# Kernel optimization log

Hardware: AMD Instinct MI355X
Metric: run time of the kernel (lower is better)

Reference implementation:

```python
import jax, jax.numpy as jnp
import numpy as np

NUM_GROUPS = 32
EPS = 1e-6


def group_norm(x, gamma, beta):
    # x: [b, c, h, w]
    b, c, h, w = x.shape
    g = NUM_GROUPS
    xg = x.reshape(b, g, c // g, h, w)
    mean = xg.mean(axis=(2, 3, 4), keepdims=True)
    var = xg.var(axis=(2, 3, 4), keepdims=True)
    xn = ((xg - mean) * jax.lax.rsqrt(var + EPS)).reshape(b, c, h, w)
    return xn * gamma[None, :, None, None] + beta[None, :, None, None]


def conv1x1(x, w, b):
    # x: [b, c, h, w], w: [out_c, in_c], b: [out_c]
    return jnp.einsum('bchw,oc->bohw', x, w) + b[None, :, None, None]


def setup_inputs() -> dict:
    key = jax.random.key(0)
    ks = jax.random.split(key, 11)
    B, C, H, W = 4, 512, 64, 64
    s = 1.0 / np.sqrt(C)
    inp = {
        'x': jax.random.normal(ks[0], (B, C, H, W), dtype=jnp.float32),
        'gn_gamma': jnp.ones((C,), dtype=jnp.float32),
        'gn_beta': jnp.zeros((C,), dtype=jnp.float32),
        'wq': jax.random.normal(ks[1], (C, C), dtype=jnp.float32) * s,
        'bq': jax.random.normal(ks[2], (C,), dtype=jnp.float32) * 0.01,
        'wk': jax.random.normal(ks[3], (C, C), dtype=jnp.float32) * s,
        'bk': jax.random.normal(ks[4], (C,), dtype=jnp.float32) * 0.01,
        'wv': jax.random.normal(ks[5], (C, C), dtype=jnp.float32) * s,
        'bv': jax.random.normal(ks[6], (C,), dtype=jnp.float32) * 0.01,
        'wo': jax.random.normal(ks[7], (C, C), dtype=jnp.float32) * s,
        'bo': jax.random.normal(ks[8], (C,), dtype=jnp.float32) * 0.01,
    }
    return inp


def reference(x, gn_gamma, gn_beta, wq, bq, wk, bk, wv, bv, wo, bo):
    b, c, h, w = x.shape
    h_ = group_norm(x, gn_gamma, gn_beta)
    q = conv1x1(h_, wq, bq).reshape(b, c, h * w)  # [b, c, n]
    k = conv1x1(h_, wk, bk).reshape(b, c, h * w)
    v = conv1x1(h_, wv, bv).reshape(b, c, h * w)
    scale = jnp.asarray(c, x.dtype) ** -0.5
    # attn[b, i, j] = softmax_j(q_i . k_j * scale)
    attn = jax.nn.softmax(jnp.einsum('bci,bcj->bij', q, k) * scale, axis=-1)
    # A[b, c, i] = sum_j attn[b, i, j] * v[b, c, j]
    A = jnp.einsum('bij,bcj->bci', attn, v).reshape(b, c, h, w)
    A = conv1x1(A, wo, bo)
    # NOTE: the original module multiplies (not adds) the input by the attention output
    return x * A
```

## Files before the change

### kernel.cpp

```cpp
#include <hip/hip_runtime.h>
#include <hip/hip_bf16.h>
#include <stdint.h>

typedef __bf16 bf16x8 __attribute__((ext_vector_type(8)));
typedef __bf16 bf16x4 __attribute__((ext_vector_type(4)));
typedef float f32x4 __attribute__((ext_vector_type(4)));

__device__ __forceinline__ void gload_lds16(const __bf16* g, __bf16* l) {
  __builtin_amdgcn_global_load_lds(
      (const __attribute__((address_space(1))) void*)g,
      (__attribute__((address_space(3))) void*)l, 16, 0, 0);
}

__global__ __launch_bounds__(256) void cvt4_kernel(const float* __restrict__ s0,
                                                   const float* __restrict__ s1,
                                                   const float* __restrict__ s2,
                                                   const float* __restrict__ s3,
                                                   __bf16* __restrict__ dst) {
  int i = blockIdx.x * 256 + threadIdx.x;
  const float* srcs[4] = {s0, s1, s2, s3};
  int m = i >> 18;
  dst[i] = (__bf16)srcs[m][i & 262143];
}

__global__ __launch_bounds__(256) void biascat_kernel(const float* __restrict__ bq,
                                                      const float* __restrict__ bk,
                                                      float* __restrict__ bqk) {
  int i = blockIdx.x * 256 + threadIdx.x;
  bqk[i] = (i < 512) ? bq[i] : bk[i - 512];
}

__global__ __launch_bounds__(256) void gn1a_kernel(const float* __restrict__ x,
                                                   __bf16* __restrict__ xbf,
                                                   float2* __restrict__ part) {
  const int tid = threadIdx.x;
  const size_t base4 = ((size_t)blockIdx.x * 8192) >> 2;
  const float4* x4 = (const float4*)x;
  bf16x4* o4 = (bf16x4*)xbf;

  float s1 = 0.f, s2 = 0.f;
#pragma unroll
  for (int j = 0; j < 8; ++j) {
    float4 t = x4[base4 + tid + j * 256];
    s1 += t.x + t.y + t.z + t.w;
    s2 += t.x * t.x + t.y * t.y + t.z * t.z + t.w * t.w;
    bf16x4 o;
    o[0] = (__bf16)t.x; o[1] = (__bf16)t.y; o[2] = (__bf16)t.z; o[3] = (__bf16)t.w;
    o4[base4 + tid + j * 256] = o;
  }
#pragma unroll
  for (int off = 32; off; off >>= 1) {
    s1 += __shfl_xor(s1, off);
    s2 += __shfl_xor(s2, off);
  }
  __shared__ float r1[4], r2[4];
  if ((tid & 63) == 0) { r1[tid >> 6] = s1; r2[tid >> 6] = s2; }
  __syncthreads();
  if (tid == 0)
    part[blockIdx.x] = float2{r1[0] + r1[1] + r1[2] + r1[3],
                              r2[0] + r2[1] + r2[2] + r2[3]};
}

__global__ __launch_bounds__(512) void gn1b_kernel(const float2* __restrict__ part,
                                                   const float* __restrict__ gamma,
                                                   const float* __restrict__ beta,
                                                   float2* __restrict__ gmbt) {
  const int b = blockIdx.x;
  const int t = threadIdx.x;
  __shared__ float sm[32], si[32];
  if (t < 32) {
    float s1 = 0.f, s2 = 0.f;
#pragma unroll
    for (int j = 0; j < 8; ++j) {
      float2 p = part[(b * 32 + t) * 8 + j];
      s1 += p.x; s2 += p.y;
    }
    const float mean = s1 * (1.f / 65536.f);
    const float var = s2 * (1.f / 65536.f) - mean * mean;
    sm[t] = mean;
    si[t] = rsqrtf(var + 1e-6f);
  }
  __syncthreads();
  const int g = t >> 4;
  const float gm = gamma[t] * si[g];
  gmbt[b * 512 + t] = float2{gm, beta[t] - sm[g] * gm};
}

__global__ __launch_bounds__(256) void gn2_kernel(const __bf16* __restrict__ xbf,
                                                  const float2* __restrict__ gmbt,
                                                  __bf16* __restrict__ hnT) {
  const int b = blockIdx.z;
  const int c0 = blockIdx.y * 64;
  const int n0 = blockIdx.x * 64;
  const int t = threadIdx.x;
  __shared__ __bf16 tile[64][72];

  {
    const int row = t >> 2;
    const int col = (t & 3) * 16;
    const __bf16* src = xbf + ((size_t)(b * 512 + c0 + row)) * 4096 + n0 + col;
    bf16x8 u0 = *(const bf16x8*)src;
    bf16x8 u1 = *(const bf16x8*)(src + 8);
    *(bf16x8*)&tile[row][col] = u0;
    *(bf16x8*)&tile[row][col + 8] = u1;
  }
  __syncthreads();
  {
    const int nrow = t >> 2;
    const int cc = (t & 3) * 16;
    bf16x8 o0, o1;
#pragma unroll
    for (int j = 0; j < 16; ++j) {
      const int c = c0 + cc + j;
      float2 s = gmbt[b * 512 + c];
      float val = (float)tile[cc + j][nrow] * s.x + s.y;
      if (j < 8) o0[j] = (__bf16)val; else o1[j - 8] = (__bf16)val;
    }
    __bf16* dst = hnT + ((size_t)b * 4096 + n0 + nrow) * 512 + c0 + cc;
    *(bf16x8*)dst = o0;
    *(bf16x8*)(dst + 8) = o1;
  }
}

__global__ __launch_bounds__(256) void softmax_bf16_kernel(__bf16* __restrict__ S) {
  const int N = 4096;
  __bf16* rp = S + (size_t)blockIdx.x * N;
  const int tid = threadIdx.x;
  bf16x8 v0 = ((const bf16x8*)rp)[tid * 2];
  bf16x8 v1 = ((const bf16x8*)rp)[tid * 2 + 1];
  float f[16];
#pragma unroll
  for (int i = 0; i < 8; ++i) { f[i] = (float)v0[i]; f[8 + i] = (float)v1[i]; }

  float mx = -1e30f;
#pragma unroll
  for (int i = 0; i < 16; ++i) mx = fmaxf(mx, f[i]);
#pragma unroll
  for (int off = 32; off; off >>= 1) mx = fmaxf(mx, __shfl_xor(mx, off));
  __shared__ float redm[4];
  if ((tid & 63) == 0) redm[tid >> 6] = mx;
  __syncthreads();
  mx = fmaxf(fmaxf(redm[0], redm[1]), fmaxf(redm[2], redm[3]));

  float sum = 0.f;
#pragma unroll
  for (int i = 0; i < 16; ++i) {
    f[i] = __expf(f[i] - mx);
    sum += f[i];
  }
#pragma unroll
  for (int off = 32; off; off >>= 1) sum += __shfl_xor(sum, off);
  __shared__ float reds[4];
  if ((tid & 63) == 0) reds[tid >> 6] = sum;
  __syncthreads();
  sum = reds[0] + reds[1] + reds[2] + reds[3];
  const float invs = 1.0f / sum;

  bf16x8 o0, o1;
#pragma unroll
  for (int i = 0; i < 8; ++i) {
    o0[i] = (__bf16)(f[i] * invs);
    o1[i] = (__bf16)(f[8 + i] * invs);
  }
  ((bf16x8*)rp)[tid * 2] = o0;
  ((bf16x8*)rp)[tid * 2 + 1] = o1;
}

template <int BN, int BIAS>
__global__ __launch_bounds__(512) void gemm8p_kernel(
    const __bf16* __restrict__ A, int lda, long long sA,
    const __bf16* __restrict__ Bm, int ldb, long long sB,
    __bf16* __restrict__ Out, int ldo, long long sO,
    const float* __restrict__ bias, float scale, int K) {
  constexpr int NF = BN / 64;
  constexpr int NH = NF / 2;
  constexpr int BSLOT = BN * 32;
  __shared__ __bf16 sm[4 * 8192 + 4 * BSLOT];
  __bf16* smB = sm + 4 * 8192;

  const int gx = gridDim.x, gxy = gx * gridDim.y;
  const int nwg = gxy * gridDim.z;
  int bid = blockIdx.x + gx * blockIdx.y + gxy * blockIdx.z;
  bid = (bid & 7) * (nwg >> 3) + (bid >> 3);
  const int bz = bid / gxy;
  const int rem = bid - bz * gxy;
  const int by = rem / gx, bx = rem - by * gx;
  const int tm0 = by * 256, tn0 = bx * BN;

  const int t = threadIdx.x;
  const int lane = t & 63, wid = t >> 6;
  const int wr = wid >> 2, wc = wid & 3;

  const __bf16* Az = A + (size_t)bz * sA;
  const __bf16* Bz = Bm + (size_t)bz * sB;

  const int scol = ((t & 3) * 8) ^ (((t >> 3) & 3) * 8);
  const __bf16* gA0 = Az + (size_t)(tm0 + (t >> 2)) * lda + scol;
  const __bf16* gA1 = gA0 + (size_t)128 * lda;
  const __bf16* gB0 = Bz + (size_t)(tn0 + (t >> 2)) * ldb + scol;
  const __bf16* gB1 = gB0 + (size_t)128 * ldb;
  __bf16* dA = sm + t * 8;
  __bf16* dB = smB + t * 8;

  auto stageA = [&](int ko, int sl) {
    gload_lds16(gA0 + ko, dA + sl * 8192);
    gload_lds16(gA1 + ko, dA + sl * 8192 + 4096);
  };
  auto stageB = [&](int ko, int sl) {
    gload_lds16(gB0 + ko, dB + sl * BSLOT);
    if constexpr (BN == 256) gload_lds16(gB1 + ko, dB + sl * BSLOT + 4096);
  };
  auto vmw = [&] {
    if constexpr (BN == 256) asm volatile("s_waitcnt vmcnt(8)" ::: "memory");
    else                     asm volatile("s_waitcnt vmcnt(6)" ::: "memory");
  };

  const int lr = lane & 15;
  const int kb = ((lane >> 4) * 16) ^ ((lr & 6) << 3);
  const __bf16* rdA = sm + (((wr * 128 + lr) * 64 + kb) >> 1);
  const __bf16* rdB = smB + (((wc * (BN / 4) + lr) * 64 + kb) >> 1);

  f32x4 acc[8][NF];
#pragma unroll
  for (int m = 0; m < 8; ++m)
#pragma unroll
    for (int n = 0; n < NF; ++n) acc[m][n] = f32x4{0.f, 0.f, 0.f, 0.f};
  bf16x8 av[8];

  auto rdAfr = [&](int sl) {
#pragma unroll
    for (int m = 0; m < 8; ++m)
      av[m] = *(const bf16x8*)(rdA + sl * 8192 + m * 512);
  };
  auto mmaPh = [&](int sl, int nh) {
    bf16x8 bv[NH];
#pragma unroll
    for (int j = 0; j < NH; ++j)
      bv[j] = *(const bf16x8*)(rdB + sl * BSLOT + (nh * NH + j) * 512);
    __builtin_amdgcn_s_barrier();
    __builtin_amdgcn_s_setprio(1);
#pragma unroll
    for (int m = 0; m < 8; ++m)
#pragma unroll
      for (int j = 0; j < NH; ++j)
        acc[m][nh * NH + j] = __builtin_amdgcn_mfma_f32_16x16x32_bf16(
            av[m], bv[j], acc[m][nh * NH + j], 0, 0, 0);
    __builtin_amdgcn_s_setprio(0);
    __builtin_amdgcn_s_barrier();
  };

  const int NT = K >> 6;
  const int NIT = NT >> 1;

  stageA(0, 0); stageB(0, 0); stageA(32, 1); stageB(32, 1);
  stageA(64, 2); stageB(64, 2);
  vmw();
  __builtin_amdgcn_s_barrier();

  for (int it = 0; it < NIT - 1; ++it) {
    const int kt = it * 2;
    const int k0 = kt * 64;
    rdAfr(0); stageA(k0 + 96, 3);          mmaPh(0, 0);
    stageB(k0 + 96, 3); vmw();             mmaPh(0, 1);
    rdAfr(1); stageA(k0 + 128, 0);         mmaPh(1, 0);
    stageB(k0 + 128, 0); vmw();            mmaPh(1, 1);
    rdAfr(2); stageA(k0 + 160, 1);         mmaPh(2, 0);
    stageB(k0 + 160, 1); vmw();            mmaPh(2, 1);
    rdAfr(3); stageA(k0 + 192, 2);         mmaPh(3, 0);
    stageB(k0 + 192, 2); vmw();            mmaPh(3, 1);
  }
  {
    const int k0 = (NT - 2) * 64;
    rdAfr(0); stageA(k0 + 96, 3);          mmaPh(0, 0);
    stageB(k0 + 96, 3); vmw();             mmaPh(0, 1);
    rdAfr(1);                              mmaPh(1, 0);
    if constexpr (BN == 256) asm volatile("s_waitcnt vmcnt(4)" ::: "memory");
    else                     asm volatile("s_waitcnt vmcnt(3)" ::: "memory");
    mmaPh(1, 1);
    rdAfr(2);                              mmaPh(2, 0);
    if constexpr (BN == 256) asm volatile("s_waitcnt vmcnt(2)" ::: "memory");
    else                     asm volatile("s_waitcnt vmcnt(1)" ::: "memory");
    mmaPh(2, 1);
    rdAfr(3);                              mmaPh(3, 0);
    mmaPh(3, 1);
  }

  const int q4 = (lane >> 4) * 4;
  const int wnb = tn0 + wc * (BN / 4);
  float bcol[NF];
#pragma unroll
  for (int n = 0; n < NF; ++n) bcol[n] = BIAS ? bias[wnb + n * 16 + lr] : 0.f;
#pragma unroll
  for (int m = 0; m < 8; ++m) {
#pragma unroll
    for (int r = 0; r < 4; ++r) {
      const int row = tm0 + wr * 128 + m * 16 + q4 + r;
      __bf16* orow = Out + (size_t)bz * sO + (size_t)row * ldo + wnb + lr;
#pragma unroll
      for (int n = 0; n < NF; ++n)
        orow[n * 16] = (__bf16)(acc[m][n][r] * scale + bcol[n]);
    }
  }
}

template <int EPI, int BIAS>
__global__ __launch_bounds__(256) void gemm_lds_kernel(
    const __bf16* __restrict__ A, int lda, long long sA,
    const __bf16* __restrict__ Bm, int ldb, long long sB,
    void* __restrict__ Out, int ldo, long long sO,
    const float* __restrict__ bias, const __bf16* __restrict__ xmul,
    long long sX, float scale, int K) {
  __shared__ __bf16 sTa[2][128 * 32];
  __shared__ __bf16 sTb[2][128 * 32];

  const int gx = gridDim.x, gxy = gx * gridDim.y;
  const int nwg = gxy * gridDim.z;
  int bid = blockIdx.x + gx * blockIdx.y + gxy * blockIdx.z;
  if ((nwg & 7) == 0) bid = (bid & 7) * (nwg >> 3) + (bid >> 3);
  const int bz = bid / gxy;
  const int rem = bid - bz * gxy;
  const int by = rem / gx;
  const int bx = rem - by * gx;

  const int tid = threadIdx.x;
  const int lane = tid & 63;
  const int wid = tid >> 6;
  const int wr = wid >> 1, wc = wid & 1;
  const int tm0 = by * 128, tn0 = bx * 128;
  const int lr = lane & 15, lk = (lane >> 4) * 8;

  const int ch0 = wid * 2;
  const int srow = lane >> 2;
  const int scol = (lane & 3) * 8;
  const __bf16* gA0 = A + (size_t)bz * sA + (size_t)(tm0 + ch0 * 16 + srow) * lda + scol;
  const __bf16* gB0 = Bm + (size_t)bz * sB + (size_t)(tn0 + ch0 * 16 + srow) * ldb + scol;
  const size_t stepA = (size_t)16 * lda, stepB = (size_t)16 * ldb;

  f32x4 acc[4][4];
#pragma unroll
  for (int i = 0; i < 4; ++i)
#pragma unroll
    for (int j = 0; j < 4; ++j) acc[i][j] = f32x4{0.f, 0.f, 0.f, 0.f};

  const int T = K >> 5;
  gload_lds16(gA0, &sTa[0][ch0 * 512]);
  gload_lds16(gA0 + stepA, &sTa[0][ch0 * 512 + 512]);
  gload_lds16(gB0, &sTb[0][ch0 * 512]);
  gload_lds16(gB0 + stepB, &sTb[0][ch0 * 512 + 512]);

  for (int tt = 0; tt < T; ++tt) {
    __syncthreads();
    const int cur = tt & 1;
    if (tt + 1 < T) {
      const __bf16* a = gA0 + (size_t)(tt + 1) * 32;
      const __bf16* b = gB0 + (size_t)(tt + 1) * 32;
      gload_lds16(a, &sTa[cur ^ 1][ch0 * 512]);
      gload_lds16(a + stepA, &sTa[cur ^ 1][ch0 * 512 + 512]);
      gload_lds16(b, &sTb[cur ^ 1][ch0 * 512]);
      gload_lds16(b + stepB, &sTb[cur ^ 1][ch0 * 512 + 512]);
    }
    const __bf16* fa = &sTa[cur][(wr * 64 + lr) * 32 + lk];
    const __bf16* fb = &sTb[cur][(wc * 64 + lr) * 32 + lk];
    bf16x8 a[4], b[4];
#pragma unroll
    for (int i = 0; i < 4; ++i) a[i] = *(const bf16x8*)(fa + i * 512);
#pragma unroll
    for (int j = 0; j < 4; ++j) b[j] = *(const bf16x8*)(fb + j * 512);
#pragma unroll
    for (int i = 0; i < 4; ++i)
#pragma unroll
      for (int j = 0; j < 4; ++j)
        acc[i][j] = __builtin_amdgcn_mfma_f32_16x16x32_bf16(a[i], b[j], acc[i][j], 0, 0, 0);
  }

  const int wm = tm0 + wr * 64, wn = tn0 + wc * 64;
#pragma unroll
  for (int i = 0; i < 4; ++i) {
#pragma unroll
    for (int r = 0; r < 4; ++r) {
      const int row = wm + i * 16 + (lane >> 4) * 4 + r;
#pragma unroll
      for (int j = 0; j < 4; ++j) {
        const int col = wn + j * 16 + lr;
        float val = acc[i][j][r] * scale;
        if (BIAS == 1) val += bias[col];
        if (BIAS == 2) val += bias[row];
        const size_t off = (size_t)bz * sO + (size_t)row * ldo + col;
        if (EPI == 0) {
          ((__bf16*)Out)[off] = (__bf16)val;
        } else if (EPI == 1) {
          ((float*)Out)[off] = val;
        } else {
          ((float*)Out)[off] = (float)xmul[(size_t)bz * sX + (size_t)row * ldo + col] * val;
        }
      }
    }
  }
}

extern "C" void kernel_launch(void* const* d_in, const int* in_sizes, int n_in,
                              void* d_out, int out_size, void* d_ws, size_t ws_size,
                              hipStream_t stream) {
  const int C = 512, N = 4096;
  const float* x = (const float*)d_in[0];
  const float* gng = (const float*)d_in[1];
  const float* gnb = (const float*)d_in[2];
  const float* wq = (const float*)d_in[3];
  const float* bq = (const float*)d_in[4];
  const float* wk = (const float*)d_in[5];
  const float* bk = (const float*)d_in[6];
  const float* wv = (const float*)d_in[7];
  const float* bv = (const float*)d_in[8];
  const float* wo = (const float*)d_in[9];
  const float* bo = (const float*)d_in[10];

  char* ws = (char*)d_ws;
  const size_t MB = 1ull << 20;
  const long long NC = (long long)N * C;
  const long long NN = (long long)N * N;
  const long long NQK = (long long)N * 1024;
  const bool batched = ws_size >= 194 * MB + 32768;

  __bf16 *S, *qkT, *a2T, *v, *xbf, *wqB;
  char* misc;
  if (batched) {
    S   = (__bf16*)(ws);
    qkT = (__bf16*)(ws + 128 * MB);
    a2T = qkT;
    v   = (__bf16*)(ws + 160 * MB);
    xbf = (__bf16*)(ws + 176 * MB);
    wqB = (__bf16*)(ws + 192 * MB);
    misc = ws + 194 * MB;
  } else {
    S   = (__bf16*)(ws);
    qkT = (__bf16*)(ws + 32 * MB);
    a2T = (__bf16*)(ws + 64 * MB);
    v   = (__bf16*)(ws + 80 * MB);
    xbf = (__bf16*)(ws + 96 * MB);
    wqB = (__bf16*)(ws + 112 * MB);
    misc = ws + 114 * MB;
  }
  __bf16* hnT = (__bf16*)ws;
  __bf16* wvB = wqB + 2 * 262144;
  __bf16* woB = wvB + 262144;
  float* bqk   = (float*)misc;
  float2* gmbt = (float2*)(misc + 4096);
  float2* part = (float2*)(misc + 20480);

  const float scl = 0.044194173824159216f;

  cvt4_kernel<<<4096, 256, 0, stream>>>(wq, wk, wv, wo, wqB);
  biascat_kernel<<<4, 256, 0, stream>>>(bq, bk, bqk);
  gn1a_kernel<<<1024, 256, 0, stream>>>(x, xbf, part);
  gn1b_kernel<<<4, 512, 0, stream>>>(part, gng, gnb, gmbt);
  gn2_kernel<<<dim3(64, 8, 4), 256, 0, stream>>>(xbf, gmbt, hnT);

  gemm8p_kernel<256, 1><<<dim3(4, 16, 4), 512, 0, stream>>>(
      hnT, C, NC, wqB, C, 0, qkT, 1024, NQK, bqk, 1.f, C);
  gemm_lds_kernel<0, 2><<<dim3(32, 4, 4), 256, 0, stream>>>(
      wvB, C, 0, hnT, C, NC, v, N, NC, bv, nullptr, 0, 1.f, C);

  if (batched) {
    gemm8p_kernel<256, 0><<<dim3(16, 16, 4), 512, 0, stream>>>(
        qkT, 1024, NQK, qkT + 512, 1024, NQK, S, N, NN, nullptr, scl, C);
    softmax_bf16_kernel<<<4 * 4096, 256, 0, stream>>>(S);
    gemm8p_kernel<128, 0><<<dim3(4, 16, 4), 512, 0, stream>>>(
        S, N, NN, v, N, NC, a2T, C, NC, nullptr, 1.f, N);
  } else {
    for (int b = 0; b < 4; ++b) {
      gemm8p_kernel<256, 0><<<dim3(16, 16, 1), 512, 0, stream>>>(
          qkT + (size_t)b * NQK, 1024, 0, qkT + (size_t)b * NQK + 512, 1024, 0,
          S, N, 0, nullptr, scl, C);
      softmax_bf16_kernel<<<4096, 256, 0, stream>>>(S);
      gemm8p_kernel<128, 0><<<dim3(4, 16, 1), 512, 0, stream>>>(
          S, N, 0, v + (size_t)b * NC, N, 0, a2T + (size_t)b * NC, C, 0,
          nullptr, 1.f, N);
    }
  }

  gemm_lds_kernel<2, 2><<<dim3(32, 4, 4), 256, 0, stream>>>(
      woB, C, 0, a2T, C, NC, (float*)d_out, N, NC, bo, xbf, NC, 1.f, C);
}
```

Baseline: 292.7 us.

## Fuse softmax into QK^T epilogue and PV prologue via partial row sums

Removes the standalone softmax kernel. The QK^T GEMM now writes raw scores plus per-tile row sums of exp (no max subtraction). A small kernel reduces these into inverse row sums, and the PV GEMM applies exp and the normalisation while loading its A fragments. The QK GEMM also loops over several M tiles per block and stages its epilogue through LDS for vectorised stores. This saves a full read and write pass over the S matrix, but it drops the max subtraction, which depends on scores staying small to avoid overflow, and it uses the output buffer as scratch.

```diff
diff --git a/kernel.cpp b/kernel.cpp
--- a/kernel.cpp
+++ b/kernel.cpp
@@ -122,60 +122,31 @@
   }
 }
 
-__global__ __launch_bounds__(256) void softmax_bf16_kernel(__bf16* __restrict__ S) {
-  const int N = 4096;
-  __bf16* rp = S + (size_t)blockIdx.x * N;
-  const int tid = threadIdx.x;
-  bf16x8 v0 = ((const bf16x8*)rp)[tid * 2];
-  bf16x8 v1 = ((const bf16x8*)rp)[tid * 2 + 1];
-  float f[16];
-#pragma unroll
-  for (int i = 0; i < 8; ++i) { f[i] = (float)v0[i]; f[8 + i] = (float)v1[i]; }
-
-  float mx = -1e30f;
-#pragma unroll
-  for (int i = 0; i < 16; ++i) mx = fmaxf(mx, f[i]);
-#pragma unroll
-  for (int off = 32; off; off >>= 1) mx = fmaxf(mx, __shfl_xor(mx, off));
-  __shared__ float redm[4];
-  if ((tid & 63) == 0) redm[tid >> 6] = mx;
-  __syncthreads();
-  mx = fmaxf(fmaxf(redm[0], redm[1]), fmaxf(redm[2], redm[3]));
-
-  float sum = 0.f;
-#pragma unroll
-  for (int i = 0; i < 16; ++i) {
-    f[i] = __expf(f[i] - mx);
-    sum += f[i];
-  }
-#pragma unroll
-  for (int off = 32; off; off >>= 1) sum += __shfl_xor(sum, off);
-  __shared__ float reds[4];
-  if ((tid & 63) == 0) reds[tid >> 6] = sum;
-  __syncthreads();
-  sum = reds[0] + reds[1] + reds[2] + reds[3];
-  const float invs = 1.0f / sum;
-
-  bf16x8 o0, o1;
-#pragma unroll
-  for (int i = 0; i < 8; ++i) {
-    o0[i] = (__bf16)(f[i] * invs);
-    o1[i] = (__bf16)(f[8 + i] * invs);
-  }
-  ((bf16x8*)rp)[tid * 2] = o0;
-  ((bf16x8*)rp)[tid * 2 + 1] = o1;
-}
-
-template <int BN, int BIAS>
+__global__ __launch_bounds__(256) void reduce_inv_kernel(const float* __restrict__ psum,
+                                                         float* __restrict__ inv) {
+  const int r = blockIdx.x * 256 + threadIdx.x;
+  const float* p = psum + (size_t)(r >> 12) * (64 * 4096) + (r & 4095);
+  float s = 0.f;
+#pragma unroll
+  for (int j = 0; j < 64; ++j) s += p[j * 4096];
+  inv[r] = 1.0f / s;
+}
+
+template <int BN, int BIAS, int NBY, int STATS, int PEXP, int KC>
 __global__ __launch_bounds__(512) void gemm8p_kernel(
     const __bf16* __restrict__ A, int lda, long long sA,
     const __bf16* __restrict__ Bm, int ldb, long long sB,
     __bf16* __restrict__ Out, int ldo, long long sO,
-    const float* __restrict__ bias, float scale, int K) {
+    const float* __restrict__ bias, float* __restrict__ pstats,
+    const float* __restrict__ rowinv, float scale) {
   constexpr int NF = BN / 64;
   constexpr int NH = NF / 2;
   constexpr int BSLOT = BN * 32;
-  __shared__ __bf16 sm[4 * 8192 + 4 * BSLOT];
+  constexpr int WN = BN / 4;
+  constexpr int BST = WN + 8;
+  constexpr int KS = KC / 32;
+  constexpr int TOTIT = (KS * NBY) / 4;
+  __shared__ __bf16 sm[4 * 8192 + 4 * BSLOT + 8 * 16 * BST];
   __bf16* smB = sm + 4 * 8192;
 
   const int gx = gridDim.x, gxy = gx * gridDim.y;
@@ -184,8 +155,8 @@
   bid = (bid & 7) * (nwg >> 3) + (bid >> 3);
   const int bz = bid / gxy;
   const int rem = bid - bz * gxy;
-  const int by = rem / gx, bx = rem - by * gx;
-  const int tm0 = by * 256, tn0 = bx * BN;
+  const int byg = rem / gx, bx = rem - byg * gx;
+  const int tn0 = bx * BN;
 
   const int t = threadIdx.x;
   const int lane = t & 63, wid = t >> 6;
@@ -195,20 +166,25 @@
   const __bf16* Bz = Bm + (size_t)bz * sB;
 
   const int scol = ((t & 3) * 8) ^ (((t >> 3) & 3) * 8);
-  const __bf16* gA0 = Az + (size_t)(tm0 + (t >> 2)) * lda + scol;
+  const __bf16* gA0 = Az + ((size_t)(byg * NBY * 256) + (t >> 2)) * lda + scol;
   const __bf16* gA1 = gA0 + (size_t)128 * lda;
   const __bf16* gB0 = Bz + (size_t)(tn0 + (t >> 2)) * ldb + scol;
   const __bf16* gB1 = gB0 + (size_t)128 * ldb;
   __bf16* dA = sm + t * 8;
   __bf16* dB = smB + t * 8;
 
-  auto stageA = [&](int ko, int sl) {
-    gload_lds16(gA0 + ko, dA + sl * 8192);
-    gload_lds16(gA1 + ko, dA + sl * 8192 + 4096);
+  auto stageA = [&](int sig) {
+    const int byT = sig / KS, ks = sig % KS;
+    const size_t off = (size_t)(byT * 256) * lda + ks * 32;
+    const int sl = sig & 3;
+    gload_lds16(gA0 + off, dA + sl * 8192);
+    gload_lds16(gA1 + off, dA + sl * 8192 + 4096);
   };
-  auto stageB = [&](int ko, int sl) {
-    gload_lds16(gB0 + ko, dB + sl * BSLOT);
-    if constexpr (BN == 256) gload_lds16(gB1 + ko, dB + sl * BSLOT + 4096);
+  auto stageB = [&](int sig) {
+    const int ks = sig % KS;
+    const int sl = sig & 3;
+    gload_lds16(gB0 + ks * 32, dB + sl * BSLOT);
+    if constexpr (BN == 256) gload_lds16(gB1 + ks * 32, dB + sl * BSLOT + 4096);
   };
   auto vmw = [&] {
     if constexpr (BN == 256) asm volatile("s_waitcnt vmcnt(8)" ::: "memory");
@@ -218,7 +194,14 @@
   const int lr = lane & 15;
   const int kb = ((lane >> 4) * 16) ^ ((lr & 6) << 3);
   const __bf16* rdA = sm + (((wr * 128 + lr) * 64 + kb) >> 1);
-  const __bf16* rdB = smB + (((wc * (BN / 4) + lr) * 64 + kb) >> 1);
+  const __bf16* rdB = smB + (((wc * WN + lr) * 64 + kb) >> 1);
+
+  float inv[8];
+  if constexpr (PEXP) {
+    const float* ip = rowinv + (size_t)bz * 4096 + byg * 256 + wr * 128 + lr;
+#pragma unroll
+    for (int m = 0; m < 8; ++m) inv[m] = ip[m * 16];
+  }
 
   f32x4 acc[8][NF];
 #pragma unroll
@@ -231,6 +214,16 @@
 #pragma unroll
     for (int m = 0; m < 8; ++m)
       av[m] = *(const bf16x8*)(rdA + sl * 8192 + m * 512);
+    if constexpr (PEXP) {
+#pragma unroll
+      for (int m = 0; m < 8; ++m) {
+        bf16x8 o;
+#pragma unroll
+        for (int e = 0; e < 8; ++e)
+          o[e] = (__bf16)(exp2f((float)av[m][e] * 1.44269504f) * inv[m]);
+        av[m] = o;
+      }
+    }
   };
   auto mmaPh = [&](int sl, int nh) {
     bf16x8 bv[NH];
@@ -249,56 +242,97 @@
     __builtin_amdgcn_s_barrier();
   };
 
-  const int NT = K >> 6;
-  const int NIT = NT >> 1;
-
-  stageA(0, 0); stageB(0, 0); stageA(32, 1); stageB(32, 1);
-  stageA(64, 2); stageB(64, 2);
+  __bf16* bnc = sm + 4 * 8192 + 4 * BSLOT + wid * 16 * BST;
+  const int q4 = (lane >> 4) * 4;
+  auto epilogue = [&](int st) {
+    const int row0 = byg * NBY * 256 + st * 256 + wr * 128;
+    const int wn = tn0 + wc * WN;
+    float bcol[NF];
+#pragma unroll
+    for (int n = 0; n < NF; ++n) bcol[n] = BIAS ? bias[wn + n * 16 + lr] : 0.f;
+    float* ps = nullptr;
+    if constexpr (STATS)
+      ps = pstats + (((size_t)bz * gx + bx) * 4 + wc) * 4096;
+#pragma unroll
+    for (int m = 0; m < 8; ++m) {
+#pragma unroll
+      for (int n = 0; n < NF; ++n)
+#pragma unroll
+        for (int r = 0; r < 4; ++r)
+          bnc[(q4 + r) * BST + n * 16 + lr] =
+              (__bf16)(acc[m][n][r] * scale + bcol[n]);
+      if constexpr (STATS) {
+#pragma unroll
+        for (int r = 0; r < 4; ++r) {
+          float s = 0.f;
+#pragma unroll
+          for (int n = 0; n < NF; ++n) {
+            float vb = (float)(__bf16)(acc[m][n][r] * scale);
+            s += exp2f(vb * 1.44269504f);
+          }
+          s += __shfl_xor(s, 1); s += __shfl_xor(s, 2);
+          s += __shfl_xor(s, 4); s += __shfl_xor(s, 8);
+          if (lr == 0) ps[row0 + m * 16 + q4 + r] = s;
+        }
+      }
+      if constexpr (WN == 64) {
+        const int rr = lane >> 3, c8 = (lane & 7) * 8;
+        bf16x8 v0 = *(const bf16x8*)&bnc[rr * BST + c8];
+        bf16x8 v1 = *(const bf16x8*)&bnc[(rr + 8) * BST + c8];
+        __bf16* op = Out + (size_t)bz * sO +
+                     (size_t)(row0 + m * 16 + rr) * ldo + wn + c8;
+        *(bf16x8*)op = v0;
+        *(bf16x8*)(op + (size_t)8 * ldo) = v1;
+      } else {
+        const int rr = lane >> 2, c8 = (lane & 3) * 8;
+        bf16x8 v0 = *(const bf16x8*)&bnc[rr * BST + c8];
+        __bf16* op = Out + (size_t)bz * sO +
+                     (size_t)(row0 + m * 16 + rr) * ldo + wn + c8;
+        *(bf16x8*)op = v0;
+      }
+    }
+  };
+
+  stageA(0); stageB(0); stageA(1); stageB(1); stageA(2); stageB(2);
   vmw();
   __builtin_amdgcn_s_barrier();
 
-  for (int it = 0; it < NIT - 1; ++it) {
-    const int kt = it * 2;
-    const int k0 = kt * 64;
-    rdAfr(0); stageA(k0 + 96, 3);          mmaPh(0, 0);
-    stageB(k0 + 96, 3); vmw();             mmaPh(0, 1);
-    rdAfr(1); stageA(k0 + 128, 0);         mmaPh(1, 0);
-    stageB(k0 + 128, 0); vmw();            mmaPh(1, 1);
-    rdAfr(2); stageA(k0 + 160, 1);         mmaPh(2, 0);
-    stageB(k0 + 160, 1); vmw();            mmaPh(2, 1);
-    rdAfr(3); stageA(k0 + 192, 2);         mmaPh(3, 0);
-    stageB(k0 + 192, 2); vmw();            mmaPh(3, 1);
-  }
-  {
-    const int k0 = (NT - 2) * 64;
-    rdAfr(0); stageA(k0 + 96, 3);          mmaPh(0, 0);
-    stageB(k0 + 96, 3); vmw();             mmaPh(0, 1);
-    rdAfr(1);                              mmaPh(1, 0);
-    if constexpr (BN == 256) asm volatile("s_waitcnt vmcnt(4)" ::: "memory");
-    else                     asm volatile("s_waitcnt vmcnt(3)" ::: "memory");
-    mmaPh(1, 1);
-    rdAfr(2);                              mmaPh(2, 0);
-    if constexpr (BN == 256) asm volatile("s_waitcnt vmcnt(2)" ::: "memory");
-    else                     asm volatile("s_waitcnt vmcnt(1)" ::: "memory");
-    mmaPh(2, 1);
-    rdAfr(3);                              mmaPh(3, 0);
-    mmaPh(3, 1);
-  }
-
-  const int q4 = (lane >> 4) * 4;
-  const int wnb = tn0 + wc * (BN / 4);
-  float bcol[NF];
-#pragma unroll
-  for (int n = 0; n < NF; ++n) bcol[n] = BIAS ? bias[wnb + n * 16 + lr] : 0.f;
-#pragma unroll
-  for (int m = 0; m < 8; ++m) {
-#pragma unroll
-    for (int r = 0; r < 4; ++r) {
-      const int row = tm0 + wr * 128 + m * 16 + q4 + r;
-      __bf16* orow = Out + (size_t)bz * sO + (size_t)row * ldo + wnb + lr;
-#pragma unroll
-      for (int n = 0; n < NF; ++n)
-        orow[n * 16] = (__bf16)(acc[m][n][r] * scale + bcol[n]);
+  int itG = 0;
+#pragma unroll 1
+  for (int st = 0; st < NBY; ++st) {
+#pragma unroll 1
+    for (int itt = 0; itt < KS / 4; ++itt, ++itG) {
+      const int s3 = 4 * itG + 3;
+      if (itG < TOTIT - 1) {
+        rdAfr(0); stageA(s3);          mmaPh(0, 0);
+        stageB(s3); vmw();             mmaPh(0, 1);
+        rdAfr(1); stageA(s3 + 1);      mmaPh(1, 0);
+        stageB(s3 + 1); vmw();         mmaPh(1, 1);
+        rdAfr(2); stageA(s3 + 2);      mmaPh(2, 0);
+        stageB(s3 + 2); vmw();         mmaPh(2, 1);
+        rdAfr(3); stageA(s3 + 3);      mmaPh(3, 0);
+        stageB(s3 + 3); vmw();         mmaPh(3, 1);
+      } else {
+        rdAfr(0); stageA(s3);          mmaPh(0, 0);
+        stageB(s3); vmw();             mmaPh(0, 1);
+        rdAfr(1);                      mmaPh(1, 0);
+        if constexpr (BN == 256) asm volatile("s_waitcnt vmcnt(4)" ::: "memory");
+        else                     asm volatile("s_waitcnt vmcnt(3)" ::: "memory");
+        mmaPh(1, 1);
+        rdAfr(2);                      mmaPh(2, 0);
+        asm volatile("s_waitcnt vmcnt(0)" ::: "memory");
+        mmaPh(2, 1);
+        rdAfr(3);                      mmaPh(3, 0);
+        mmaPh(3, 1);
+      }
+    }
+    epilogue(st);
+    if (st + 1 < NBY) {
+      asm volatile("s_waitcnt vmcnt(0)" ::: "memory");
+#pragma unroll
+      for (int m = 0; m < 8; ++m)
+#pragma unroll
+        for (int n = 0; n < NF; ++n) acc[m][n] = f32x4{0.f, 0.f, 0.f, 0.f};
     }
   }
 }
@@ -446,6 +480,8 @@
   float* bqk   = (float*)misc;
   float2* gmbt = (float2*)(misc + 4096);
   float2* part = (float2*)(misc + 20480);
+  float* psum   = (float*)d_out;
+  float* rowInv = (float*)d_out + 64 * 4096 * 4;
 
   const float scl = 0.044194173824159216f;
 
@@ -455,26 +491,26 @@
   gn1b_kernel<<<4, 512, 0, stream>>>(part, gng, gnb, gmbt);
   gn2_kernel<<<dim3(64, 8, 4), 256, 0, stream>>>(xbf, gmbt, hnT);
 
-  gemm8p_kernel<256, 1><<<dim3(4, 16, 4), 512, 0, stream>>>(
-      hnT, C, NC, wqB, C, 0, qkT, 1024, NQK, bqk, 1.f, C);
+  gemm8p_kernel<256, 1, 1, 0, 0, 512><<<dim3(4, 16, 4), 512, 0, stream>>>(
+      hnT, C, NC, wqB, C, 0, qkT, 1024, NQK, bqk, nullptr, nullptr, 1.f);
   gemm_lds_kernel<0, 2><<<dim3(32, 4, 4), 256, 0, stream>>>(
       wvB, C, 0, hnT, C, NC, v, N, NC, bv, nullptr, 0, 1.f, C);
 
   if (batched) {
-    gemm8p_kernel<256, 0><<<dim3(16, 16, 4), 512, 0, stream>>>(
-        qkT, 1024, NQK, qkT + 512, 1024, NQK, S, N, NN, nullptr, scl, C);
-    softmax_bf16_kernel<<<4 * 4096, 256, 0, stream>>>(S);
-    gemm8p_kernel<128, 0><<<dim3(4, 16, 4), 512, 0, stream>>>(
-        S, N, NN, v, N, NC, a2T, C, NC, nullptr, 1.f, N);
+    gemm8p_kernel<256, 0, 4, 1, 0, 512><<<dim3(16, 4, 4), 512, 0, stream>>>(
+        qkT, 1024, NQK, qkT + 512, 1024, NQK, S, N, NN, nullptr, psum, nullptr, scl);
+    reduce_inv_kernel<<<64, 256, 0, stream>>>(psum, rowInv);
+    gemm8p_kernel<128, 0, 1, 0, 1, 4096><<<dim3(4, 16, 4), 512, 0, stream>>>(
+        S, N, NN, v, N, NC, a2T, C, NC, nullptr, nullptr, rowInv, 1.f);
   } else {
     for (int b = 0; b < 4; ++b) {
-      gemm8p_kernel<256, 0><<<dim3(16, 16, 1), 512, 0, stream>>>(
+      gemm8p_kernel<256, 0, 4, 1, 0, 512><<<dim3(16, 4, 1), 512, 0, stream>>>(
           qkT + (size_t)b * NQK, 1024, 0, qkT + (size_t)b * NQK + 512, 1024, 0,
-          S, N, 0, nullptr, scl, C);
-      softmax_bf16_kernel<<<4096, 256, 0, stream>>>(S);
-      gemm8p_kernel<128, 0><<<dim3(4, 16, 1), 512, 0, stream>>>(
+          S, N, 0, nullptr, psum, nullptr, scl);
+      reduce_inv_kernel<<<16, 256, 0, stream>>>(psum, rowInv);
+      gemm8p_kernel<128, 0, 1, 0, 1, 4096><<<dim3(4, 16, 1), 512, 0, stream>>>(
           S, N, 0, v + (size_t)b * NC, N, 0, a2T + (size_t)b * NC, C, 0,
-          nullptr, 1.f, N);
+          nullptr, nullptr, rowInv, 1.f);
     }
   }
 
```

Result: slower. 928.7 us (+217.3%).
